# Kernel tuning notes

Hardware: AMD Instinct MI355X
Metric: run time of the kernel (lower is better)

## Reference

```python
import jax, jax.numpy as jnp
import numpy as np

EPSILON = 1.5  # quality-tolerance threshold from init_kwargs
NEG_INF = -1000000000.0


def setup_inputs() -> dict:
    key = jax.random.key(0)
    k1, k2, k3 = jax.random.split(key, 3)
    B, S, D, E = 4, 4096, 2048, 64
    return {
        "hidden_states": jax.random.normal(k1, (B, S, D), dtype=jnp.float32),
        "gate_W": jax.random.normal(k2, (E, D), dtype=jnp.float32),  # nn.Linear weight [out,in]
        "secret_projection": jax.random.normal(k3, (D, E), dtype=jnp.float32),
        "top_k": 2,
    }


def reference(hidden_states, gate_W, secret_projection, top_k):
    # raw gate logits: Linear without bias -> x @ W^T
    raw_logits = jnp.einsum("bsd,ed->bse", hidden_states, gate_W)
    # watermark bias via secret LSH projection
    watermark_bias = jnp.einsum("bsd,de->bse", hidden_states, secret_projection)
    # indifference zone: experts whose logit is within epsilon of the max
    max_logits = jnp.max(raw_logits, axis=-1, keepdims=True)
    safe_mask = raw_logits >= max_logits - EPSILON
    modified_scores = jnp.where(safe_mask, watermark_bias, jnp.asarray(NEG_INF, raw_logits.dtype))
    # top-k over watermark-preferred safe experts
    _, selected_experts = jax.lax.top_k(modified_scores, top_k)
    # gather original logits at selected experts, softmax over the k slots
    router_logits = jnp.take_along_axis(raw_logits, selected_experts, axis=-1)
    routing_weights = jax.nn.softmax(router_logits, axis=-1)
    return routing_weights, selected_experts
```

## Files before the change

kernel.cpp:

```cpp
#include <hip/hip_runtime.h>
#include <stdint.h>


#define DDIM 2048
#define NEXP 64
#define TOKB 128
#define KSPL 4
#define NTS  16
#define NEG_INF  -1000000000.0f
#define MRG_RAW  0.04f
#define MRG_WM   0.15f

typedef __attribute__((ext_vector_type(8))) short bf16x8;
typedef __attribute__((ext_vector_type(4))) float f32x4;

union BFrag { bf16x8 v; uint32_t w[4]; uint4 q; };

__device__ inline void split8_rne(const float* a, bf16x8* hi, bf16x8* lo) {
    BFrag h, l;
    #pragma unroll
    for (int p = 0; p < 4; ++p) {
        const uint32_t u0 = __float_as_uint(a[2*p]);
        const uint32_t u1 = __float_as_uint(a[2*p+1]);
        const uint32_t h0 = (u0 + 0x7FFFu + ((u0 >> 16) & 1u)) >> 16;
        const uint32_t h1 = (u1 + 0x7FFFu + ((u1 >> 16) & 1u)) >> 16;
        const float r0 = a[2*p]   - __uint_as_float(h0 << 16);
        const float r1 = a[2*p+1] - __uint_as_float(h1 << 16);
        const uint32_t v0 = __float_as_uint(r0);
        const uint32_t v1 = __float_as_uint(r1);
        const uint32_t l0 = (v0 + 0x7FFFu + ((v0 >> 16) & 1u)) >> 16;
        const uint32_t l1 = (v1 + 0x7FFFu + ((v1 >> 16) & 1u)) >> 16;
        h.w[p] = h0 | (h1 << 16);
        l.w[p] = l0 | (l1 << 16);
    }
    *hi = h.v; *lo = l.v;
}

__device__ inline void split8t(const float* a, bf16x8* hi, bf16x8* lo) {
    BFrag h, l;
    #pragma unroll
    for (int p = 0; p < 4; ++p) {
        const uint32_t u0 = __float_as_uint(a[2*p]);
        const uint32_t u1 = __float_as_uint(a[2*p+1]);
        h.w[p] = (u0 >> 16) | (u1 & 0xFFFF0000u);
        const float r0 = a[2*p]   - __uint_as_float(u0 & 0xFFFF0000u);
        const float r1 = a[2*p+1] - __uint_as_float(u1 & 0xFFFF0000u);
        l.w[p] = (__float_as_uint(r0) >> 16) | (__float_as_uint(r1) & 0xFFFF0000u);
    }
    *hi = h.v; *lo = l.v;
}

__global__ void prep_b(const float* __restrict__ gateW, const float* __restrict__ secret,
                       uint4* __restrict__ wsB) {
    const int kstep = blockIdx.x;
    const int s = threadIdx.x >> 6;
    const int l = threadIdx.x & 63;
    const int col = s * 16 + (l & 15);
    const int kb  = kstep * 32 + (l >> 4) * 8;
    float v[8];
    if (col < NEXP) {
        #pragma unroll
        for (int j = 0; j < 8; ++j) v[j] = gateW[(size_t)col * DDIM + kb + j];
    } else {
        #pragma unroll
        for (int j = 0; j < 8; ++j) v[j] = secret[(size_t)(kb + j) * NEXP + (col - NEXP)];
    }
    bf16x8 hi, lo; split8_rne(v, &hi, &lo);
    const size_t base = (size_t)(kstep * 8 + s) * 128 + l;
    BFrag t;
    t.v = hi; wsB[base]      = t.q;
    t.v = lo; wsB[base + 64] = t.q;
}

__device__ inline void gl_lds16(const char* g, char* l) {
    __builtin_amdgcn_global_load_lds(
        (const __attribute__((address_space(1))) void*)g,
        (__attribute__((address_space(3))) void*)l, 16, 0, 0);
}

__global__ __launch_bounds__(512, 4)
void gemm_p(const float* __restrict__ x, const char* __restrict__ wsB,
            float* __restrict__ wsP, int ntok)
{
    __shared__ __align__(16) char lds[2][32768];

    const int tid = threadIdx.x;
    const int w = tid >> 6, l = tid & 63;
    const int c = l & 15;
    const int g = l >> 4;
    const int q  = blockIdx.x & (KSPL - 1);
    const int mb = blockIdx.x / KSPL;
    const int rowbase = mb * TOKB;
    const int wrow = rowbase + w * 16;

    f32x4 acc[8];
    #pragma unroll
    for (int s = 0; s < 8; ++s) acc[s] = (f32x4){0.f, 0.f, 0.f, 0.f};

    const char*  bq = wsB + (size_t)(q * NTS) * 16384;
    const float* xq = x + q * (DDIM / KSPL);

    #define STAGE(ts, buf)                                                         \
        {                                                                          \
            _Pragma("unroll")                                                      \
            for (int j = 0; j < 2; ++j) {                                          \
                const int slot = j * 512 + tid;                                    \
                const int i = slot >> 6;                                           \
                gl_lds16(bq + (size_t)(ts) * 16384 + i * 1024 + l * 16,            \
                         &lds[buf][slot * 16]);                                    \
            }                                                                      \
            _Pragma("unroll")                                                      \
            for (int j = 0; j < 2; ++j) {                                          \
                const int a = j * 512 + tid;                                       \
                const int r = a >> 3, cg = a & 7;                                  \
                const int scg = cg ^ (r & 7);                                      \
                gl_lds16((const char*)(xq + (size_t)(rowbase + r) * DDIM           \
                                       + (ts) * 32 + scg * 4),                     \
                         &lds[buf][16384 + a * 16]);                               \
            }                                                                      \
        }

    STAGE(0, 0);
    asm volatile("s_waitcnt vmcnt(0)" ::: "memory");
    __builtin_amdgcn_s_barrier();

    #pragma unroll 1
    for (int ts = 0; ts < NTS; ++ts) {
        const int cur = ts & 1;
        const int nts = (ts + 1 < NTS) ? ts + 1 : ts;
        STAGE(nts, cur ^ 1);

        const char* ab = &lds[cur][16384];
        const int r = w * 16 + c;
        const int s0 = (2 * g)     ^ (r & 7);
        const int s1 = (2 * g + 1) ^ (r & 7);
        const float4 fa = *reinterpret_cast<const float4*>(ab + r * 128 + s0 * 16);
        const float4 fb = *reinterpret_cast<const float4*>(ab + r * 128 + s1 * 16);
        const float va[8] = {fa.x, fa.y, fa.z, fa.w, fb.x, fb.y, fb.z, fb.w};
        bf16x8 ah, al;
        split8t(va, &ah, &al);

        const char* bb = lds[cur];
        #pragma unroll
        for (int s = 0; s < 8; ++s) {
            const bf16x8 bh = *reinterpret_cast<const bf16x8*>(bb + (2*s)     * 1024 + l * 16);
            const bf16x8 bl = *reinterpret_cast<const bf16x8*>(bb + (2*s + 1) * 1024 + l * 16);
            acc[s] = __builtin_amdgcn_mfma_f32_16x16x32_bf16(ah, bh, acc[s], 0, 0, 0);
            acc[s] = __builtin_amdgcn_mfma_f32_16x16x32_bf16(ah, bl, acc[s], 0, 0, 0);
            acc[s] = __builtin_amdgcn_mfma_f32_16x16x32_bf16(al, bh, acc[s], 0, 0, 0);
        }

        asm volatile("s_waitcnt vmcnt(0)" ::: "memory");
        __builtin_amdgcn_s_barrier();
    }
    #undef STAGE

    const size_t MN = (size_t)ntok * 128;
    #pragma unroll
    for (int s = 0; s < 8; ++s)
        #pragma unroll
        for (int r = 0; r < 4; ++r)
            wsP[(size_t)q * MN + (size_t)(wrow + g * 4 + r) * 128 + s * 16 + c] = acc[s][r];
}

template <int KSPLIT>
__global__ __launch_bounds__(256, 4)
void router_k(const float* __restrict__ wsP,
              const float* __restrict__ x,
              const float* __restrict__ gateW,
              const float* __restrict__ secret,
              float* __restrict__ out, int ntok)
{
    const int t = blockIdx.x * 4 + (threadIdx.x >> 6);
    const int e = threadIdx.x & 63;
    const size_t MN = (size_t)ntok * 128;

    float raw = 0.f, wm = 0.f;
    #pragma unroll
    for (int q = 0; q < KSPLIT; ++q) {
        raw += wsP[(size_t)q * MN + (size_t)t * 128 + e];
        wm  += wsP[(size_t)q * MN + (size_t)t * 128 + NEXP + e];
    }

    float rmax = raw;
    #pragma unroll
    for (int off = 32; off; off >>= 1) rmax = fmaxf(rmax, __shfl_xor(rmax, off));

    if (__any(fabsf(raw - (rmax - 1.5f)) < MRG_RAW)) {
        float s0 = 0.f, s1 = 0.f, s2 = 0.f, s3 = 0.f;
        const float4* xr = reinterpret_cast<const float4*>(x + (size_t)t * DDIM);
        const float4* wr = reinterpret_cast<const float4*>(gateW + (size_t)e * DDIM);
        for (int k = 0; k < DDIM / 4; ++k) {
            const float4 a = xr[k], b = wr[k];
            s0 = fmaf(a.x, b.x, s0); s1 = fmaf(a.y, b.y, s1);
            s2 = fmaf(a.z, b.z, s2); s3 = fmaf(a.w, b.w, s3);
        }
        raw = (s0 + s1) + (s2 + s3);
        rmax = raw;
        #pragma unroll
        for (int off = 32; off; off >>= 1) rmax = fmaxf(rmax, __shfl_xor(rmax, off));
    }

    const bool safe = (raw >= rmax - 1.5f);
    float m = safe ? wm : NEG_INF;

    float v1 = m; int e1 = e;
    #pragma unroll
    for (int off = 32; off; off >>= 1) {
        const float ov = __shfl_xor(v1, off); const int oi = __shfl_xor(e1, off);
        if (ov > v1 || (ov == v1 && oi < e1)) { v1 = ov; e1 = oi; }
    }
    float v2 = (e == e1) ? -3.0e38f : m; int e2 = e;
    #pragma unroll
    for (int off = 32; off; off >>= 1) {
        const float ov = __shfl_xor(v2, off); const int oi = __shfl_xor(e2, off);
        if (ov > v2 || (ov == v2 && oi < e2)) { v2 = ov; e2 = oi; }
    }
    float v3 = (e == e1 || e == e2) ? -3.0e38f : m; int e3 = e;
    #pragma unroll
    for (int off = 32; off; off >>= 1) {
        const float ov = __shfl_xor(v3, off); const int oi = __shfl_xor(e3, off);
        if (ov > v3 || (ov == v3 && oi < e3)) { v3 = ov; e3 = oi; }
    }

    const bool wmRisk = (v2 > NEG_INF + 1.0f && v1 - v2 < MRG_WM) ||
                        (v3 > NEG_INF + 1.0f && v2 - v3 < MRG_WM);
    if (__any(wmRisk)) {
        float s0 = 0.f, s1 = 0.f, s2 = 0.f, s3 = 0.f;
        const float* xr = x + (size_t)t * DDIM;
        for (int k = 0; k < DDIM; k += 4) {
            s0 = fmaf(xr[k + 0], secret[(size_t)(k + 0) * NEXP + e], s0);
            s1 = fmaf(xr[k + 1], secret[(size_t)(k + 1) * NEXP + e], s1);
            s2 = fmaf(xr[k + 2], secret[(size_t)(k + 2) * NEXP + e], s2);
            s3 = fmaf(xr[k + 3], secret[(size_t)(k + 3) * NEXP + e], s3);
        }
        m = safe ? ((s0 + s1) + (s2 + s3)) : NEG_INF;
        v1 = m; e1 = e;
        #pragma unroll
        for (int off = 32; off; off >>= 1) {
            const float ov = __shfl_xor(v1, off); const int oi = __shfl_xor(e1, off);
            if (ov > v1 || (ov == v1 && oi < e1)) { v1 = ov; e1 = oi; }
        }
        v2 = (e == e1) ? -3.0e38f : m; e2 = e;
        #pragma unroll
        for (int off = 32; off; off >>= 1) {
            const float ov = __shfl_xor(v2, off); const int oi = __shfl_xor(e2, off);
            if (ov > v2 || (ov == v2 && oi < e2)) { v2 = ov; e2 = oi; }
        }
    }

    const float l1 = __shfl(raw, e1);
    const float l2 = __shfl(raw, e2);

    if (e == 0) {
        const float mm = fmaxf(l1, l2);
        const float x1 = expf(l1 - mm), x2 = expf(l2 - mm);
        const float inv = 1.0f / (x1 + x2);
        out[(size_t)t * 2 + 0] = x1 * inv;
        out[(size_t)t * 2 + 1] = x2 * inv;
        out[(size_t)2 * ntok + t * 2 + 0] = (float)e1;
        out[(size_t)2 * ntok + t * 2 + 1] = (float)e2;
    }
}

extern "C" void kernel_launch(void* const* d_in, const int* in_sizes, int n_in,
                              void* d_out, int out_size, void* d_ws, size_t ws_size,
                              hipStream_t stream) {
    const float* x      = (const float*)d_in[0];
    const float* gateW  = (const float*)d_in[1];
    const float* secret = (const float*)d_in[2];
    float* out = (float*)d_out;

    const int ntok = in_sizes[0] / DDIM;
    uint4* wsB = (uint4*)d_ws;
    float* wsP = (float*)((char*)d_ws + (2u << 20));

    prep_b<<<64, 512, 0, stream>>>(gateW, secret, wsB);
    gemm_p<<<(ntok / TOKB) * KSPL, 512, 0, stream>>>(x, (const char*)wsB, wsP, ntok);
    router_k<KSPL><<<ntok / 4, 256, 0, stream>>>(wsP, x, gateW, secret, out, ntok);
}
```

Before: 94.86 us.

## Halve token tile, use 256-thread blocks with partial waitcnt pipelining

```diff
diff --git a/kernel.cpp b/kernel.cpp
--- a/kernel.cpp
+++ b/kernel.cpp
@@ -4,7 +4,7 @@
 
 #define DDIM 2048
 #define NEXP 64
-#define TOKB 128
+#define TOKB 64
 #define KSPL 4
 #define NTS  16
 #define NEG_INF  -1000000000.0f
@@ -14,7 +14,7 @@
 typedef __attribute__((ext_vector_type(8))) short bf16x8;
 typedef __attribute__((ext_vector_type(4))) float f32x4;
 
-union BFrag { bf16x8 v; uint32_t w[4]; uint4 q; };
+union BFrag { bf16x8 v; f32x4 f; uint32_t w[4]; uint4 q; };
 
 __device__ inline void split8_rne(const float* a, bf16x8* hi, bf16x8* lo) {
     BFrag h, l;
@@ -78,11 +78,17 @@
         (__attribute__((address_space(3))) void*)l, 16, 0, 0);
 }
 
-__global__ __launch_bounds__(512, 4)
-void gemm_p(const float* __restrict__ x, const char* __restrict__ wsB,
+__device__ inline f32x4 ds128(unsigned addr) {
+    f32x4 r;
+    asm volatile("ds_read_b128 %0, %1" : "=v"(r) : "v"(addr));
+    return r;
+}
+
+__global__ __launch_bounds__(256, 3)
+void gemm_c(const float* __restrict__ x, const char* __restrict__ wsB,
             float* __restrict__ wsP, int ntok)
 {
-    __shared__ __align__(16) char lds[2][32768];
+    __shared__ __align__(16) char lds[2][24576];
 
     const int tid = threadIdx.x;
     const int w = tid >> 6, l = tid & 63;
@@ -103,15 +109,14 @@
     #define STAGE(ts, buf)                                                         \
         {                                                                          \
             _Pragma("unroll")                                                      \
-            for (int j = 0; j < 2; ++j) {                                          \
-                const int slot = j * 512 + tid;                                    \
-                const int i = slot >> 6;                                           \
-                gl_lds16(bq + (size_t)(ts) * 16384 + i * 1024 + l * 16,            \
+            for (int j = 0; j < 4; ++j) {                                          \
+                const int slot = j * 256 + tid;                                    \
+                gl_lds16(bq + (size_t)(ts) * 16384 + slot * 16,                    \
                          &lds[buf][slot * 16]);                                    \
             }                                                                      \
             _Pragma("unroll")                                                      \
             for (int j = 0; j < 2; ++j) {                                          \
-                const int a = j * 512 + tid;                                       \
+                const int a = j * 256 + tid;                                       \
                 const int r = a >> 3, cg = a & 7;                                  \
                 const int scg = cg ^ (r & 7);                                      \
                 gl_lds16((const char*)(xq + (size_t)(rowbase + r) * DDIM           \
@@ -121,36 +126,47 @@
         }
 
     STAGE(0, 0);
-    asm volatile("s_waitcnt vmcnt(0)" ::: "memory");
-    __builtin_amdgcn_s_barrier();
 
     #pragma unroll 1
     for (int ts = 0; ts < NTS; ++ts) {
         const int cur = ts & 1;
-        const int nts = (ts + 1 < NTS) ? ts + 1 : ts;
-        STAGE(nts, cur ^ 1);
-
-        const char* ab = &lds[cur][16384];
+        if (ts + 1 < NTS) {
+            STAGE(ts + 1, cur ^ 1);
+            asm volatile("s_waitcnt vmcnt(6)" ::: "memory");
+        } else {
+            asm volatile("s_waitcnt vmcnt(0)" ::: "memory");
+        }
+        __builtin_amdgcn_s_barrier();
+
+        const unsigned bb = (unsigned)(size_t)&lds[cur][0];
+
         const int r = w * 16 + c;
-        const int s0 = (2 * g)     ^ (r & 7);
-        const int s1 = (2 * g + 1) ^ (r & 7);
-        const float4 fa = *reinterpret_cast<const float4*>(ab + r * 128 + s0 * 16);
-        const float4 fb = *reinterpret_cast<const float4*>(ab + r * 128 + s1 * 16);
-        const float va[8] = {fa.x, fa.y, fa.z, fa.w, fb.x, fb.y, fb.z, fb.w};
+        const unsigned arow = bb + 16384u + (unsigned)(r * 128);
+        BFrag fa, fb;
+        fa.f = ds128(arow + (unsigned)((( 2 * g)     ^ (r & 7)) * 16));
+        fb.f = ds128(arow + (unsigned)(((2 * g + 1) ^ (r & 7)) * 16));
+        BFrag bf[16];
+        #pragma unroll
+        for (int i = 0; i < 16; ++i)
+            bf[i].f = ds128(bb + (unsigned)(i * 1024 + l * 16));
+
+        asm volatile("s_waitcnt lgkmcnt(0)" ::: "memory");
+        __builtin_amdgcn_sched_barrier(0);
+
+        const float va[8] = {fa.f[0], fa.f[1], fa.f[2], fa.f[3],
+                             fb.f[0], fb.f[1], fb.f[2], fb.f[3]};
         bf16x8 ah, al;
         split8t(va, &ah, &al);
 
-        const char* bb = lds[cur];
+        __builtin_amdgcn_s_setprio(1);
         #pragma unroll
         for (int s = 0; s < 8; ++s) {
-            const bf16x8 bh = *reinterpret_cast<const bf16x8*>(bb + (2*s)     * 1024 + l * 16);
-            const bf16x8 bl = *reinterpret_cast<const bf16x8*>(bb + (2*s + 1) * 1024 + l * 16);
-            acc[s] = __builtin_amdgcn_mfma_f32_16x16x32_bf16(ah, bh, acc[s], 0, 0, 0);
-            acc[s] = __builtin_amdgcn_mfma_f32_16x16x32_bf16(ah, bl, acc[s], 0, 0, 0);
-            acc[s] = __builtin_amdgcn_mfma_f32_16x16x32_bf16(al, bh, acc[s], 0, 0, 0);
-        }
-
-        asm volatile("s_waitcnt vmcnt(0)" ::: "memory");
+            acc[s] = __builtin_amdgcn_mfma_f32_16x16x32_bf16(ah, bf[2*s].v,     acc[s], 0, 0, 0);
+            acc[s] = __builtin_amdgcn_mfma_f32_16x16x32_bf16(ah, bf[2*s + 1].v, acc[s], 0, 0, 0);
+            acc[s] = __builtin_amdgcn_mfma_f32_16x16x32_bf16(al, bf[2*s].v,     acc[s], 0, 0, 0);
+        }
+        __builtin_amdgcn_s_setprio(0);
+
         __builtin_amdgcn_s_barrier();
     }
     #undef STAGE
@@ -276,6 +292,6 @@
     float* wsP = (float*)((char*)d_ws + (2u << 20));
 
     prep_b<<<64, 512, 0, stream>>>(gateW, secret, wsB);
-    gemm_p<<<(ntok / TOKB) * KSPL, 512, 0, stream>>>(x, (const char*)wsB, wsP, ntok);
+    gemm_c<<<(ntok / TOKB) * KSPL, 256, 0, stream>>>(x, (const char*)wsB, wsP, ntok);
     router_k<KSPL><<<ntok / 4, 256, 0, stream>>>(wsP, x, gateW, secret, out, ntok);
 }
```

Result: slower. 99.40 us (+4.8%).
